# Kernel optimization log

Measured on AMD Instinct MI355X. Metric: run time of the kernel, lower is better.

## Reference

```python
import jax, jax.numpy as jnp
import numpy as np
import math

B, S, D, H = 4, 2048, 1024, 16
DH = D // H  # 64
DFF = 4 * D
EPS = 1e-5


def layer_norm(x, g, b):
    mu = jnp.mean(x, axis=-1, keepdims=True)
    var = jnp.mean(jnp.square(x - mu), axis=-1, keepdims=True)
    return (x - mu) * jax.lax.rsqrt(var + EPS) * g + b


def apply_rope(xq, xk, freqs_cis):
    # xq, xk: [B, S, H, DH]; freqs_cis: [S, DH//2, 2] (cos, sin)
    cos = freqs_cis[None, :, None, :, 0]  # [1, S, 1, DH//2]
    sin = freqs_cis[None, :, None, :, 1]

    def rot(t):
        tr = t.reshape(*t.shape[:-1], DH // 2, 2)
        t0, t1 = tr[..., 0], tr[..., 1]
        o0 = t0 * cos - t1 * sin
        o1 = t0 * sin + t1 * cos
        return jnp.stack([o0, o1], axis=-1).reshape(t.shape)

    return rot(xq), rot(xk)


def setup_inputs() -> dict:
    key = jax.random.key(0)
    ks = jax.random.split(key, 12)
    x = jax.random.normal(ks[0], (B, S, D), dtype=jnp.float32)
    # rotary frequencies (theta = 10000), stored as (cos, sin)
    inv = 1.0 / (10000.0 ** (np.arange(0, DH, 2, dtype=np.float32) / DH))
    t = np.arange(S, dtype=np.float32)
    ang = np.outer(t, inv)  # [S, DH//2]
    freqs_cis = jnp.asarray(np.stack([np.cos(ang), np.sin(ang)], axis=-1))
    s = 1.0 / math.sqrt(D)
    sf = 1.0 / math.sqrt(DFF)
    return {
        "x": x,
        "freqs_cis": freqs_cis,
        "wq": jax.random.normal(ks[1], (D, D), dtype=jnp.float32) * s,
        "wk": jax.random.normal(ks[2], (D, D), dtype=jnp.float32) * s,
        "wv": jax.random.normal(ks[3], (D, D), dtype=jnp.float32) * s,
        "w_proj": jax.random.normal(ks[4], (D, D), dtype=jnp.float32) * s,
        "b_proj": jnp.zeros((D,), dtype=jnp.float32),
        "w_ff1": jax.random.normal(ks[5], (D, DFF), dtype=jnp.float32) * s,
        "b_ff1": jnp.zeros((DFF,), dtype=jnp.float32),
        "w_ff2": jax.random.normal(ks[6], (DFF, D), dtype=jnp.float32) * sf,
        "b_ff2": jnp.zeros((D,), dtype=jnp.float32),
        "ln1_g": jnp.ones((D,), dtype=jnp.float32),
        "ln1_b": jnp.zeros((D,), dtype=jnp.float32),
        "ln2_g": jnp.ones((D,), dtype=jnp.float32),
        "ln2_b": jnp.zeros((D,), dtype=jnp.float32),
    }


def reference(x, freqs_cis, wq, wk, wv, w_proj, b_proj, w_ff1, b_ff1, w_ff2,
              b_ff2, ln1_g, ln1_b, ln2_g, ln2_b):
    # --- attention block (pre-norm) ---
    h = layer_norm(x, ln1_g, ln1_b)
    xq = (h @ wq).reshape(B, S, H, DH)
    xk = (h @ wk).reshape(B, S, H, DH)
    xv = (h @ wv).reshape(B, S, H, DH)
    xq, xk = apply_rope(xq, xk, freqs_cis)
    # [B, H, S, S]
    att = jnp.einsum("bqhd,bkhd->bhqk", xq, xk) / math.sqrt(DH)
    att = jax.nn.softmax(att, axis=-1)
    out = jnp.einsum("bhqk,bkhd->bqhd", att, xv).reshape(B, S, D)
    x = x + out @ w_proj + b_proj
    # --- feed-forward block (pre-norm, GELU) ---
    h2 = layer_norm(x, ln2_g, ln2_b)
    ff = jax.nn.gelu(h2 @ w_ff1 + b_ff1, approximate=False) @ w_ff2 + b_ff2
    return x + ff
```

## Files before the change

kernel.cpp:

```cpp
#include <hip/hip_runtime.h>
#include <hip/hip_bf16.h>


#define Bb_ 4
#define Ss_ 2048
#define Dd_ 1024
#define Hh_ 16
#define DFF_ 4096

typedef __bf16 bf16x8 __attribute__((ext_vector_type(8)));
typedef float f32x4 __attribute__((ext_vector_type(4)));

static __device__ __forceinline__ unsigned short f2bf(float f) {
  union { float f; unsigned u; } v; v.f = f;
  unsigned r = v.u + 0x7FFF + ((v.u >> 16) & 1);
  return (unsigned short)(r >> 16);
}
static __device__ __forceinline__ float bf2f(unsigned short h) {
  union { unsigned u; float f; } v; v.u = ((unsigned)h) << 16;
  return v.f;
}
static __device__ __forceinline__ unsigned cvt_pk_bf16(float lo, float hi) {
  unsigned r;
  asm("v_cvt_pk_bf16_f32 %0, %1, %2" : "=v"(r) : "v"(lo), "v"(hi));
  return r;
}

static __device__ __forceinline__ void gl16(const unsigned short* g, unsigned short* l) {
  __builtin_amdgcn_global_load_lds(
      (const __attribute__((address_space(1))) void*)g,
      (__attribute__((address_space(3))) void*)l, 16, 0, 0);
}

__global__ __launch_bounds__(256) void ln_kernel(
    const float* __restrict__ x, const float* __restrict__ g,
    const float* __restrict__ bb, unsigned short* __restrict__ out)
{
  const int row = blockIdx.x;
  const int t = threadIdx.x;
  const float4 v = reinterpret_cast<const float4*>(x + (size_t)row * Dd_)[t];
  float s = v.x + v.y + v.z + v.w;
  float ss = v.x*v.x + v.y*v.y + v.z*v.z + v.w*v.w;
  #pragma unroll
  for (int o = 32; o; o >>= 1) { s += __shfl_down(s, o); ss += __shfl_down(ss, o); }
  __shared__ float red[8];
  if ((t & 63) == 0) { red[t >> 6] = s; red[4 + (t >> 6)] = ss; }
  __syncthreads();
  s = red[0] + red[1] + red[2] + red[3];
  ss = red[4] + red[5] + red[6] + red[7];
  const float mean = s * (1.f / Dd_);
  const float var = ss * (1.f / Dd_) - mean * mean;
  const float inv = rsqrtf(var + 1e-5f);
  const float4 gv = reinterpret_cast<const float4*>(g)[t];
  const float4 bv = reinterpret_cast<const float4*>(bb)[t];
  ushort4 o4;
  o4.x = f2bf((v.x - mean) * inv * gv.x + bv.x);
  o4.y = f2bf((v.y - mean) * inv * gv.y + bv.y);
  o4.z = f2bf((v.z - mean) * inv * gv.z + bv.z);
  o4.w = f2bf((v.w - mean) * inv * gv.w + bv.w);
  reinterpret_cast<ushort4*>(out + (size_t)row * Dd_)[t] = o4;
}

__global__ __launch_bounds__(256) void tconv_kernel(
    const float* __restrict__ src, unsigned short* __restrict__ dst, int K, int N)
{
  __shared__ float tile[32][33];
  const int bx = blockIdx.x, by = blockIdx.y;
  const int tx = threadIdx.x & 31, ty = threadIdx.x >> 5;
  #pragma unroll
  for (int i = 0; i < 4; i++)
    tile[ty + i * 8][tx] = src[(size_t)(by * 32 + ty + i * 8) * N + bx * 32 + tx];
  __syncthreads();
  #pragma unroll
  for (int i = 0; i < 4; i++)
    dst[(size_t)(bx * 32 + ty + i * 8) * K + by * 32 + tx] = f2bf(tile[tx][ty + i * 8]);
}

__global__ __launch_bounds__(256) void rope_kernel(
    unsigned short* __restrict__ qkv, const float* __restrict__ fc)
{
  const int c = blockIdx.x * 256 + threadIdx.x;
  const int row = c >> 8;
  const int rem = c & 255;
  const int qk = rem >> 7;
  const int e8 = rem & 127;
  const int s = row & (Ss_ - 1);
  const float4 f0 = *reinterpret_cast<const float4*>(fc + s * 64 + (e8 & 7) * 8);
  const float4 f1 = *reinterpret_cast<const float4*>(fc + s * 64 + (e8 & 7) * 8 + 4);
  unsigned short* p = qkv + (size_t)row * 3072 + qk * 1024 + e8 * 8;
  uint4 dv = *reinterpret_cast<const uint4*>(p);
  unsigned u[4] = {dv.x, dv.y, dv.z, dv.w};
  const float cs[8] = {f0.x, f0.y, f0.z, f0.w, f1.x, f1.y, f1.z, f1.w};
  #pragma unroll
  for (int j = 0; j < 4; j++) {
    const float t0 = bf2f((unsigned short)(u[j] & 0xffff));
    const float t1 = bf2f((unsigned short)(u[j] >> 16));
    const float cj = cs[2 * j], sj = cs[2 * j + 1];
    const float o0 = t0 * cj - t1 * sj;
    const float o1 = t0 * sj + t1 * cj;
    u[j] = (unsigned)f2bf(o0) | ((unsigned)f2bf(o1) << 16);
  }
  uint4 ov; ov.x = u[0]; ov.y = u[1]; ov.z = u[2]; ov.w = u[3];
  *reinterpret_cast<uint4*>(p) = ov;
}

__global__ __launch_bounds__(256) void vtrans_kernel(
    const unsigned short* __restrict__ qkv, unsigned short* __restrict__ vt)
{
  __shared__ unsigned short tile[64 * 64];
  const int st = blockIdx.x, h = blockIdx.y, b = blockIdx.z;
  const int t = threadIdx.x;
  const unsigned short* src = qkv + (size_t)(b * Ss_ + st * 64) * 3072 + 2048 + h * 64;
  {
    const int s = t >> 2;
    const int v = (s >> 3) & 7;
    #pragma unroll
    for (int j = 0; j < 2; j++) {
      const int col8 = (t & 3) * 2 + j;
      const uint4 d = *reinterpret_cast<const uint4*>(src + (size_t)s * 3072 + col8 * 8);
      *reinterpret_cast<uint4*>(&tile[s * 64 + ((col8 * 8) ^ (v * 8))]) = d;
    }
  }
  __syncthreads();
  unsigned short* dst = vt + (size_t)((b * 16 + h) * 64) * Ss_ + st * 64;
  #pragma unroll
  for (int it = 0; it < 2; it++) {
    const int c = t + it * 256;
    const int d = c >> 3, s8 = c & 7;
    unsigned short o[8];
    #pragma unroll
    for (int j = 0; j < 8; j++) {
      const int s = s8 * 8 + j;
      o[j] = tile[s * 64 + (d ^ (((s >> 3) & 7) * 8))];
    }
    *reinterpret_cast<uint4*>(dst + (size_t)d * Ss_ + s8 * 8) = *reinterpret_cast<uint4*>(o);
  }
}

template<int MODE>
__global__ __launch_bounds__(256) void gemm_kernel(
    const unsigned short* __restrict__ A,
    const unsigned short* __restrict__ BT,
    int K, int nbn, int N,
    const float* __restrict__ bias,
    const float* __restrict__ resid,
    void* __restrict__ out)
{
  __shared__ unsigned short As[2][128 * 64];
  __shared__ unsigned short Bs[2][128 * 64];
  const int t = threadIdx.x;

  const int nwg = gridDim.x;
  const int id = blockIdx.x;
  const int sid = (id & 7) * (nwg >> 3) + (id >> 3);
  const int bm = sid / nbn, bn = sid % nbn;

  const int w = t >> 6, lane = t & 63;
  const int lq = lane >> 4, lr = lane & 15;
  const int wm = (w >> 1) * 64, wn = (w & 1) * 64;
  const int srow = t >> 3, sg8 = t & 7;
  const int sw8 = sg8 ^ (srow & 7);

  const unsigned short* Ab = A + (size_t)(bm * 128) * K;
  const unsigned short* Bb = BT + (size_t)(bn * 128) * K;

  f32x4 acc[4][4] = {};
  const int nt = K >> 6;

  auto stage = [&](int tt, int rb) {
    const unsigned short* as = Ab + (size_t)srow * K + tt * 64 + sw8 * 8;
    unsigned short* ad = &As[rb][srow * 64 + sg8 * 8];
    const unsigned short* bs = Bb + (size_t)srow * K + tt * 64 + sw8 * 8;
    unsigned short* bd = &Bs[rb][srow * 64 + sg8 * 8];
    #pragma unroll
    for (int i = 0; i < 4; i++) {
      gl16(as + (size_t)(i * 32) * K, ad + i * 32 * 64);
      gl16(bs + (size_t)(i * 32) * K, bd + i * 32 * 64);
    }
  };

  stage(0, 0);
  __syncthreads();

  int cur = 0;
  for (int t0 = 0; t0 < nt; ++t0) {
    if (t0 + 1 < nt) stage(t0 + 1, cur ^ 1);
    const unsigned short* Ar = As[cur];
    const unsigned short* Br = Bs[cur];
    __builtin_amdgcn_s_setprio(1);
    #pragma unroll
    for (int kc = 0; kc < 2; kc++) {
      const int cofs = kc * 32 + lq * 8;
      const int csw = (lr & 7) * 8;
      bf16x8 af[4], bfr[4];
      #pragma unroll
      for (int i = 0; i < 4; i++) {
        af[i]  = *reinterpret_cast<const bf16x8*>(&Ar[(wm + i * 16 + lr) * 64 + (cofs ^ csw)]);
        bfr[i] = *reinterpret_cast<const bf16x8*>(&Br[(wn + i * 16 + lr) * 64 + (cofs ^ csw)]);
      }
      #pragma unroll
      for (int i = 0; i < 4; i++)
        #pragma unroll
        for (int j = 0; j < 4; j++)
          acc[i][j] = __builtin_amdgcn_mfma_f32_16x16x32_bf16(af[i], bfr[j], acc[i][j], 0, 0, 0);
    }
    __builtin_amdgcn_s_setprio(0);
    __syncthreads();
    cur ^= 1;
  }

  const int growbase = bm * 128 + wm + lq * 4;
  const int gcolbase = bn * 128 + wn + lr;
  #pragma unroll
  for (int j = 0; j < 4; j++) {
    const int col = gcolbase + j * 16;
    const float bj = (MODE != 0) ? bias[col] : 0.f;
    #pragma unroll
    for (int i = 0; i < 4; i++) {
      #pragma unroll
      for (int r = 0; r < 4; r++) {
        const int grow = growbase + i * 16 + r;
        const float v = acc[i][j][r];
        if (MODE == 0) {
          ((unsigned short*)out)[(size_t)grow * N + col] = f2bf(v);
        } else if (MODE == 1 || MODE == 3) {
          ((float*)out)[(size_t)grow * N + col] = v + bj + resid[(size_t)grow * N + col];
        } else {
          const float u = v + bj;
          const float gel = 0.5f * u * (1.f + erff(u * 0.70710678118654752f));
          ((unsigned short*)out)[(size_t)grow * N + col] = f2bf(gel);
        }
      }
    }
  }
}

__global__ __launch_bounds__(256) void attn_kernel(
    const unsigned short* __restrict__ qkv,
    const unsigned short* __restrict__ vt,
    unsigned short* __restrict__ attout)
{
  __shared__ unsigned short Ks[2][64 * 64];
  __shared__ unsigned short Vs[2][64 * 64];
  __shared__ unsigned short Ps[128 * 64];
  const int qt = blockIdx.x, h = blockIdx.y, b = blockIdx.z;
  const int t = threadIdx.x, w = t >> 6, lane = t & 63;
  const int lq = lane >> 4, lr = lane & 15;
  const int srow = t >> 3, sg8 = t & 7;

  const unsigned short* kg = qkv + (size_t)(b * Ss_) * 3072 + 1024 + h * 64;
  const unsigned short* vg = vt + (size_t)((b * 16 + h) * 64) * Ss_;

  bf16x8 aq[2][2];
  {
    const unsigned short* qg = qkv + (size_t)(b * Ss_ + qt * 128) * 3072 + h * 64;
    #pragma unroll
    for (int mt = 0; mt < 2; mt++)
      #pragma unroll
      for (int kc = 0; kc < 2; kc++)
        aq[mt][kc] = *reinterpret_cast<const bf16x8*>(
            qg + (size_t)(w * 32 + mt * 16 + lr) * 3072 + kc * 32 + lq * 8);
  }

  bf16x8 ones;
  #pragma unroll
  for (int j = 0; j < 8; j++) ones[j] = (__bf16)1.0f;

  f32x4 oacc[2][4] = {};
  f32x4 ssum[2] = {};

  const int g8s0 = sg8 ^ ((srow)      & 7);
  const int g8s1 = sg8 ^ ((srow + 32) & 7);

  {
    gl16(kg + (size_t)(srow)      * 3072 + g8s0 * 8, &Ks[0][(srow)      * 64 + sg8 * 8]);
    gl16(kg + (size_t)(srow + 32) * 3072 + g8s1 * 8, &Ks[0][(srow + 32) * 64 + sg8 * 8]);
    gl16(vg + (size_t)(srow)      * Ss_  + g8s0 * 8, &Vs[0][(srow)      * 64 + sg8 * 8]);
    gl16(vg + (size_t)(srow + 32) * Ss_  + g8s1 * 8, &Vs[0][(srow + 32) * 64 + sg8 * 8]);
  }
  __syncthreads();

  const float SC2 = 0.125f * 1.44269504088896f;

  for (int kt = 0; kt < Ss_ / 64; ++kt) {
    const int cur = kt & 1;
    if (kt < Ss_ / 64 - 1) {
      const int nb = cur ^ 1;
      const size_t ko = (size_t)((kt + 1) * 64);
      gl16(kg + (ko + srow)      * 3072 + g8s0 * 8, &Ks[nb][(srow)      * 64 + sg8 * 8]);
      gl16(kg + (ko + srow + 32) * 3072 + g8s1 * 8, &Ks[nb][(srow + 32) * 64 + sg8 * 8]);
      gl16(vg + (size_t)(srow)      * Ss_ + (kt + 1) * 64 + g8s0 * 8, &Vs[nb][(srow)      * 64 + sg8 * 8]);
      gl16(vg + (size_t)(srow + 32) * Ss_ + (kt + 1) * 64 + g8s1 * 8, &Vs[nb][(srow + 32) * 64 + sg8 * 8]);
    }

    f32x4 sacc[2][4] = {};
    #pragma unroll
    for (int kc = 0; kc < 2; kc++) {
      const int cofs = kc * 32 + lq * 8;
      const int swz = (lr & 7) * 8;
      bf16x8 kb[4];
      #pragma unroll
      for (int nf = 0; nf < 4; nf++)
        kb[nf] = *reinterpret_cast<const bf16x8*>(&Ks[cur][(nf * 16 + lr) * 64 + (cofs ^ swz)]);
      #pragma unroll
      for (int mt = 0; mt < 2; mt++)
        #pragma unroll
        for (int nf = 0; nf < 4; nf++)
          sacc[mt][nf] = __builtin_amdgcn_mfma_f32_16x16x32_bf16(kb[nf], aq[mt][kc], sacc[mt][nf], 0, 0, 0);
    }

    #pragma unroll
    for (int mt = 0; mt < 2; mt++) {
      const int qrow = w * 32 + mt * 16 + lr;
      char* prow = reinterpret_cast<char*>(Ps) + qrow * 128;
      const int sw = (lr & 7) << 4;
      #pragma unroll
      for (int nf = 0; nf < 4; nf++) {
        const float p0 = __builtin_amdgcn_exp2f(sacc[mt][nf][0] * SC2);
        const float p1 = __builtin_amdgcn_exp2f(sacc[mt][nf][1] * SC2);
        const float p2 = __builtin_amdgcn_exp2f(sacc[mt][nf][2] * SC2);
        const float p3 = __builtin_amdgcn_exp2f(sacc[mt][nf][3] * SC2);
        uint2 pw;
        pw.x = cvt_pk_bf16(p0, p1);
        pw.y = cvt_pk_bf16(p2, p3);
        *reinterpret_cast<uint2*>(prow + ((nf * 32 + lq * 8) ^ sw)) = pw;
      }
    }

    #pragma unroll
    for (int kc = 0; kc < 2; kc++) {
      const int cofs = kc * 32 + lq * 8;
      const int swz = (lr & 7) * 8;
      bf16x8 pa[2], vb[4];
      #pragma unroll
      for (int mt = 0; mt < 2; mt++) {
        const int qrow = w * 32 + mt * 16 + lr;
        pa[mt] = *reinterpret_cast<const bf16x8*>(
            reinterpret_cast<const char*>(Ps) + qrow * 128 + ((kc * 64 + lq * 16) ^ ((lr & 7) << 4)));
      }
      #pragma unroll
      for (int mt = 0; mt < 2; mt++)
        ssum[mt] = __builtin_amdgcn_mfma_f32_16x16x32_bf16(pa[mt], ones, ssum[mt], 0, 0, 0);
      #pragma unroll
      for (int nf = 0; nf < 4; nf++)
        vb[nf] = *reinterpret_cast<const bf16x8*>(&Vs[cur][(nf * 16 + lr) * 64 + (cofs ^ swz)]);
      #pragma unroll
      for (int mt = 0; mt < 2; mt++)
        #pragma unroll
        for (int nf = 0; nf < 4; nf++)
          oacc[mt][nf] = __builtin_amdgcn_mfma_f32_16x16x32_bf16(pa[mt], vb[nf], oacc[mt][nf], 0, 0, 0);
    }

    __syncthreads();
  }

  #pragma unroll
  for (int mt = 0; mt < 2; mt++) {
    #pragma unroll
    for (int r = 0; r < 4; r++) {
      const float inv = 1.f / ssum[mt][r];
      const int grow = b * Ss_ + qt * 128 + w * 32 + mt * 16 + lq * 4 + r;
      #pragma unroll
      for (int nf = 0; nf < 4; nf++)
        attout[(size_t)grow * Dd_ + h * 64 + nf * 16 + lr] = f2bf(oacc[mt][nf][r] * inv);
    }
  }
}

extern "C" void kernel_launch(void* const* d_in, const int* in_sizes, int n_in,
                              void* d_out, int out_size, void* d_ws, size_t ws_size,
                              hipStream_t stream) {
  const float* x      = (const float*)d_in[0];
  const float* fc     = (const float*)d_in[1];
  const float* wq     = (const float*)d_in[2];
  const float* wk     = (const float*)d_in[3];
  const float* wv     = (const float*)d_in[4];
  const float* w_proj = (const float*)d_in[5];
  const float* b_proj = (const float*)d_in[6];
  const float* w_ff1  = (const float*)d_in[7];
  const float* b_ff1  = (const float*)d_in[8];
  const float* w_ff2  = (const float*)d_in[9];
  const float* b_ff2  = (const float*)d_in[10];
  const float* ln1_g  = (const float*)d_in[11];
  const float* ln1_b  = (const float*)d_in[12];
  const float* ln2_g  = (const float*)d_in[13];
  const float* ln2_b  = (const float*)d_in[14];

  char* ws = (char*)d_ws;
  unsigned short* hb     = (unsigned short*)(ws);
  unsigned short* wqkvT  = (unsigned short*)(ws + 16777216ull);
  unsigned short* wprojT = (unsigned short*)(ws + 23068672ull);
  unsigned short* wff1T  = (unsigned short*)(ws + 25165824ull);
  unsigned short* wff2T  = (unsigned short*)(ws + 33554432ull);
  float*          x2     = (float*)(ws + 41943040ull);
  unsigned short* vtb    = (unsigned short*)(ws + 41943040ull);
  unsigned short* attoutb= (unsigned short*)(ws + 75497472ull);
  unsigned short* qkvb   = (unsigned short*)(ws + 92274688ull);
  unsigned short* ff1b   = qkvb;

  dim3 blk(256);

  tconv_kernel<<<dim3(32, 32), blk, 0, stream>>>(wq, wqkvT, 1024, 1024);
  tconv_kernel<<<dim3(32, 32), blk, 0, stream>>>(wk, wqkvT + 1024 * 1024, 1024, 1024);
  tconv_kernel<<<dim3(32, 32), blk, 0, stream>>>(wv, wqkvT + 2 * 1024 * 1024, 1024, 1024);
  tconv_kernel<<<dim3(32, 32), blk, 0, stream>>>(w_proj, wprojT, 1024, 1024);
  tconv_kernel<<<dim3(128, 32), blk, 0, stream>>>(w_ff1, wff1T, 1024, 4096);
  tconv_kernel<<<dim3(32, 128), blk, 0, stream>>>(w_ff2, wff2T, 4096, 1024);

  ln_kernel<<<8192, blk, 0, stream>>>(x, ln1_g, ln1_b, hb);
  gemm_kernel<0><<<1536, blk, 0, stream>>>(hb, wqkvT, 1024, 24, 3072, nullptr, nullptr, qkvb);
  rope_kernel<<<8192, blk, 0, stream>>>(qkvb, fc);
  vtrans_kernel<<<dim3(32, 16, 4), blk, 0, stream>>>(qkvb, vtb);
  attn_kernel<<<dim3(16, 16, 4), blk, 0, stream>>>(qkvb, vtb, attoutb);
  gemm_kernel<1><<<512, blk, 0, stream>>>(attoutb, wprojT, 1024, 8, 1024, b_proj, x, x2);
  ln_kernel<<<8192, blk, 0, stream>>>(x2, ln2_g, ln2_b, hb);
  gemm_kernel<2><<<2048, blk, 0, stream>>>(hb, wff1T, 1024, 32, 4096, b_ff1, nullptr, ff1b);
  gemm_kernel<3><<<512, blk, 0, stream>>>(ff1b, wff2T, 4096, 8, 1024, b_ff2, x2, (float*)d_out);
}
```

Baseline: 440.9 us.

## Enlarge GEMM tiles to 256xBN with 512 threads and deeper async pipeline

The GEMM moves from a 128x128 tile with 256 threads to a 256x256 (or 256x128) tile with 512 threads and 8 waves. Each wave computes a 128xBN/4 sub-tile. The loop now keeps two tiles in flight, using explicit vmcnt waits and raw barriers so global-to-LDS loads overlap the MFMA work. Larger tiles raise arithmetic intensity and cut global traffic, but they use more LDS (up to 128KB) and more registers. The N=1024 GEMMs launch only 256 blocks, which may underfill the GPU.

```diff
diff --git a/kernel.cpp b/kernel.cpp
--- a/kernel.cpp
+++ b/kernel.cpp
@@ -26,7 +26,7 @@
   return r;
 }
 
-static __device__ __forceinline__ void gl16(const unsigned short* g, unsigned short* l) {
+static __device__ __forceinline__ void gl16(const unsigned short* g, void* l) {
   __builtin_amdgcn_global_load_lds(
       (const __attribute__((address_space(1))) void*)g,
       (__attribute__((address_space(3))) void*)l, 16, 0, 0);
@@ -137,8 +137,8 @@
   }
 }
 
-template<int MODE>
-__global__ __launch_bounds__(256) void gemm_kernel(
+template<int MODE, int BN>
+__global__ __launch_bounds__(512, 2) void gemm_kernel(
     const unsigned short* __restrict__ A,
     const unsigned short* __restrict__ BT,
     int K, int nbn, int N,
@@ -146,8 +146,11 @@
     const float* __restrict__ resid,
     void* __restrict__ out)
 {
-  __shared__ unsigned short As[2][128 * 64];
-  __shared__ unsigned short Bs[2][128 * 64];
+  constexpr int NF = BN / 64;
+  constexpr int ABYTES = 256 * 64 * 2;
+  constexpr int BBYTES = BN * 64 * 2;
+  __shared__ __align__(16) unsigned short As[2][256 * 64];
+  __shared__ __align__(16) unsigned short Bs[2][BN * 64];
   const int t = threadIdx.x;
 
   const int nwg = gridDim.x;
@@ -157,66 +160,99 @@
 
   const int w = t >> 6, lane = t & 63;
   const int lq = lane >> 4, lr = lane & 15;
-  const int wm = (w >> 1) * 64, wn = (w & 1) * 64;
+  const int wr = w >> 2, wc = w & 3;
   const int srow = t >> 3, sg8 = t & 7;
   const int sw8 = sg8 ^ (srow & 7);
 
-  const unsigned short* Ab = A + (size_t)(bm * 128) * K;
-  const unsigned short* Bb = BT + (size_t)(bn * 128) * K;
-
-  f32x4 acc[4][4] = {};
+  const unsigned short* ag = A  + (size_t)(bm * 256 + srow) * K + sw8 * 8;
+  const unsigned short* bg = BT + (size_t)(bn * BN  + srow) * K + sw8 * 8;
+
+  char* AsB = (char*)As;
+  char* BsB = (char*)Bs;
+  const int csw = (lr & 7) * 8;
+  int aoff[2], boff[2];
+  aoff[0] = (wr * 128 + lr) * 128 + 2 * ((lq * 8) ^ csw);
+  aoff[1] = (wr * 128 + lr) * 128 + 2 * ((32 + lq * 8) ^ csw);
+  boff[0] = (wc * (BN / 4) + lr) * 128 + 2 * ((lq * 8) ^ csw);
+  boff[1] = (wc * (BN / 4) + lr) * 128 + 2 * ((32 + lq * 8) ^ csw);
+  const int sdst = (srow * 64 + sg8 * 8) * 2;
+
+  f32x4 acc[8][NF] = {};
   const int nt = K >> 6;
 
-  auto stage = [&](int tt, int rb) {
-    const unsigned short* as = Ab + (size_t)srow * K + tt * 64 + sw8 * 8;
-    unsigned short* ad = &As[rb][srow * 64 + sg8 * 8];
-    const unsigned short* bs = Bb + (size_t)srow * K + tt * 64 + sw8 * 8;
-    unsigned short* bd = &Bs[rb][srow * 64 + sg8 * 8];
-    #pragma unroll
-    for (int i = 0; i < 4; i++) {
-      gl16(as + (size_t)(i * 32) * K, ad + i * 32 * 64);
-      gl16(bs + (size_t)(i * 32) * K, bd + i * 32 * 64);
-    }
-  };
-
-  stage(0, 0);
-  __syncthreads();
-
-  int cur = 0;
-  for (int t0 = 0; t0 < nt; ++t0) {
-    if (t0 + 1 < nt) stage(t0 + 1, cur ^ 1);
-    const unsigned short* Ar = As[cur];
-    const unsigned short* Br = Bs[cur];
-    __builtin_amdgcn_s_setprio(1);
-    #pragma unroll
-    for (int kc = 0; kc < 2; kc++) {
-      const int cofs = kc * 32 + lq * 8;
-      const int csw = (lr & 7) * 8;
-      bf16x8 af[4], bfr[4];
-      #pragma unroll
-      for (int i = 0; i < 4; i++) {
-        af[i]  = *reinterpret_cast<const bf16x8*>(&Ar[(wm + i * 16 + lr) * 64 + (cofs ^ csw)]);
-        bfr[i] = *reinterpret_cast<const bf16x8*>(&Br[(wn + i * 16 + lr) * 64 + (cofs ^ csw)]);
-      }
-      #pragma unroll
-      for (int i = 0; i < 4; i++)
-        #pragma unroll
-        for (int j = 0; j < 4; j++)
-          acc[i][j] = __builtin_amdgcn_mfma_f32_16x16x32_bf16(af[i], bfr[j], acc[i][j], 0, 0, 0);
-    }
-    __builtin_amdgcn_s_setprio(0);
-    __syncthreads();
-    cur ^= 1;
-  }
-
-  const int growbase = bm * 128 + wm + lq * 4;
-  const int gcolbase = bn * 128 + wn + lr;
-  #pragma unroll
-  for (int j = 0; j < 4; j++) {
+#define STAGE8(TT, D)                                                         \
+  {                                                                           \
+    const size_t co_ = (size_t)(TT) * 64;                                     \
+    _Pragma("unroll")                                                         \
+    for (int i_ = 0; i_ < 4; i_++)                                            \
+      gl16(ag + (size_t)(i_ * 64) * K + co_, AsB + (D) * ABYTES + sdst + i_ * 8192); \
+    _Pragma("unroll")                                                         \
+    for (int i_ = 0; i_ < NF; i_++)                                           \
+      gl16(bg + (size_t)(i_ * 64) * K + co_, BsB + (D) * BBYTES + sdst + i_ * 8192); \
+  }
+
+#define READS8(D, KC)                                                         \
+  {                                                                           \
+    _Pragma("unroll")                                                         \
+    for (int i_ = 0; i_ < 8; i_++)                                            \
+      af[i_] = *reinterpret_cast<const bf16x8*>(AsB + (D) * ABYTES + aoff[KC] + i_ * 2048); \
+    _Pragma("unroll")                                                         \
+    for (int j_ = 0; j_ < NF; j_++)                                           \
+      bf[j_] = *reinterpret_cast<const bf16x8*>(BsB + (D) * BBYTES + boff[KC] + j_ * 2048); \
+  }
+
+#define MFMA8()                                                               \
+  {                                                                           \
+    __builtin_amdgcn_s_setprio(1);                                            \
+    _Pragma("unroll")                                                         \
+    for (int i_ = 0; i_ < 8; i_++)                                            \
+      _Pragma("unroll")                                                       \
+      for (int j_ = 0; j_ < NF; j_++)                                         \
+        acc[i_][j_] = __builtin_amdgcn_mfma_f32_16x16x32_bf16(af[i_], bf[j_], acc[i_][j_], 0, 0, 0); \
+    __builtin_amdgcn_s_setprio(0);                                            \
+  }
+
+#define BODY8(U, D)                                                           \
+  {                                                                           \
+    if ((U) + 1 < nt) {                                                       \
+      if constexpr (BN == 256) asm volatile("s_waitcnt vmcnt(8)" ::: "memory"); \
+      else                     asm volatile("s_waitcnt vmcnt(6)" ::: "memory"); \
+    } else {                                                                  \
+      asm volatile("s_waitcnt vmcnt(0)" ::: "memory");                        \
+    }                                                                         \
+    __builtin_amdgcn_sched_barrier(0);                                        \
+    __builtin_amdgcn_s_barrier();                                             \
+    bf16x8 af[8], bf[NF];                                                     \
+    READS8(D, 0);                                                             \
+    MFMA8();                                                                  \
+    READS8(D, 1);                                                             \
+    asm volatile("s_waitcnt lgkmcnt(0)" ::: "memory");                        \
+    __builtin_amdgcn_sched_barrier(0);                                        \
+    __builtin_amdgcn_s_barrier();                                             \
+    if ((U) + 2 < nt) STAGE8((U) + 2, D);                                     \
+    MFMA8();                                                                  \
+  }
+
+  STAGE8(0, 0);
+  STAGE8(1, 1);
+
+  for (int u = 0; u < nt; u += 2) {
+    BODY8(u, 0);
+    BODY8(u + 1, 1);
+  }
+#undef STAGE8
+#undef READS8
+#undef MFMA8
+#undef BODY8
+
+  const int growbase = bm * 256 + wr * 128 + lq * 4;
+  const int gcolbase = bn * BN + wc * (BN / 4) + lr;
+  #pragma unroll
+  for (int j = 0; j < NF; j++) {
     const int col = gcolbase + j * 16;
     const float bj = (MODE != 0) ? bias[col] : 0.f;
     #pragma unroll
-    for (int i = 0; i < 4; i++) {
+    for (int i = 0; i < 8; i++) {
       #pragma unroll
       for (int r = 0; r < 4; r++) {
         const int grow = growbase + i * 16 + r;
@@ -399,6 +435,7 @@
   unsigned short* ff1b   = qkvb;
 
   dim3 blk(256);
+  dim3 blk512(512);
 
   tconv_kernel<<<dim3(32, 32), blk, 0, stream>>>(wq, wqkvT, 1024, 1024);
   tconv_kernel<<<dim3(32, 32), blk, 0, stream>>>(wk, wqkvT + 1024 * 1024, 1024, 1024);
@@ -408,12 +445,12 @@
   tconv_kernel<<<dim3(32, 128), blk, 0, stream>>>(w_ff2, wff2T, 4096, 1024);
 
   ln_kernel<<<8192, blk, 0, stream>>>(x, ln1_g, ln1_b, hb);
-  gemm_kernel<0><<<1536, blk, 0, stream>>>(hb, wqkvT, 1024, 24, 3072, nullptr, nullptr, qkvb);
+  gemm_kernel<0, 256><<<384, blk512, 0, stream>>>(hb, wqkvT, 1024, 12, 3072, nullptr, nullptr, qkvb);
   rope_kernel<<<8192, blk, 0, stream>>>(qkvb, fc);
   vtrans_kernel<<<dim3(32, 16, 4), blk, 0, stream>>>(qkvb, vtb);
   attn_kernel<<<dim3(16, 16, 4), blk, 0, stream>>>(qkvb, vtb, attoutb);
-  gemm_kernel<1><<<512, blk, 0, stream>>>(attoutb, wprojT, 1024, 8, 1024, b_proj, x, x2);
+  gemm_kernel<1, 128><<<256, blk512, 0, stream>>>(attoutb, wprojT, 1024, 8, 1024, b_proj, x, x2);
   ln_kernel<<<8192, blk, 0, stream>>>(x2, ln2_g, ln2_b, hb);
-  gemm_kernel<2><<<2048, blk, 0, stream>>>(hb, wff1T, 1024, 32, 4096, b_ff1, nullptr, ff1b);
-  gemm_kernel<3><<<512, blk, 0, stream>>>(ff1b, wff2T, 4096, 8, 1024, b_ff2, x2, (float*)d_out);
-}
+  gemm_kernel<2, 256><<<512, blk512, 0, stream>>>(hb, wff1T, 1024, 16, 4096, b_ff1, nullptr, ff1b);
+  gemm_kernel<3, 128><<<256, blk512, 0, stream>>>(ff1b, wff2T, 4096, 8, 1024, b_ff2, x2, (float*)d_out);
+}
```

After: 733.6 us. 66.4% more time.
